# Kernel optimization log

Measured on AMD Instinct MI355X. Metric: run time of the kernel, lower is better.

## Reference

```python
import jax, jax.numpy as jnp
import numpy as np
import math

B, S, D, H, L, V, DFF = 16, 512, 1024, 16, 12, 32000, 4096
DK = D // H
MASK_ID = 1
LN_EPS = 1e-5


def _positional_encoding(seq_len, d):
    pos = np.arange(seq_len, dtype=np.float32)[:, None]
    div = np.exp(np.arange(0, d, 2, dtype=np.float32) * -(math.log(10000.0) / d))
    pe = np.zeros((seq_len, d), dtype=np.float32)
    pe[:, 0::2] = np.sin(pos * div)
    pe[:, 1::2] = np.cos(pos * div)
    return jnp.asarray(pe)


def _layernorm(x, scale, bias):
    mu = jnp.mean(x, axis=-1, keepdims=True)
    var = jnp.mean(jnp.square(x - mu), axis=-1, keepdims=True)
    return (x - mu) * jax.lax.rsqrt(var + LN_EPS) * scale + bias


def setup_inputs() -> dict:
    key = jax.random.key(0)
    ks = jax.random.split(key, 10)
    masked = jax.random.randint(ks[0], (B, S), 0, V, dtype=jnp.int32)
    tok_emb = jax.random.normal(ks[1], (V, D), dtype=jnp.float32) * 0.02
    tok_emb = tok_emb.at[0].set(0.0)  # padding_idx=0 row is zero
    seg_emb = jax.random.normal(ks[2], (3, D), dtype=jnp.float32) * 0.02
    return {
        "masked": masked,
        "tok_emb": tok_emb,
        "seg_emb": seg_emb,
        "ln1_scale": jnp.ones((L, D), jnp.float32),
        "ln1_bias": jnp.zeros((L, D), jnp.float32),
        "wq": jax.random.normal(ks[3], (L, D, D), dtype=jnp.float32) * 0.02,
        "bq": jnp.zeros((L, D), jnp.float32),
        "wo": jax.random.normal(ks[4], (L, D, D), dtype=jnp.float32) * 0.02,
        "bo": jnp.zeros((L, D), jnp.float32),
        "ln2_scale": jnp.ones((L, D), jnp.float32),
        "ln2_bias": jnp.zeros((L, D), jnp.float32),
        "w1": jax.random.normal(ks[5], (L, D, DFF), dtype=jnp.float32) * 0.02,
        "b1": jnp.zeros((L, DFF), jnp.float32),
        "w2": jax.random.normal(ks[6], (L, DFF, D), dtype=jnp.float32) * 0.02,
        "b2": jnp.zeros((L, D), jnp.float32),
    }


def reference(masked, tok_emb, seg_emb, ln1_scale, ln1_bias, wq, bq, wo, bo,
              ln2_scale, ln2_bias, w1, b1, w2, b2):
    pe = _positional_encoding(S, D)
    # segment_labels are forced to all-ones in the source forward
    x = tok_emb[masked] + pe[None, :, :] + seg_emb[1][None, None, :]  # [B,S,D]
    # pad mask built from (input != mask_id) as in source; broadcast over queries
    key_ok = (masked != MASK_ID)  # [B,S]
    attn_bias = jnp.where(key_ok[:, None, None, :], 0.0, -1e9)  # [B,1,1,S]
    scale = 1.0 / math.sqrt(DK)
    for l in range(L):
        xn = _layernorm(x, ln1_scale[l], ln1_bias[l])
        # NOTE: source uses q_linear for q, k and v -> single projection t
        t = (xn @ wq[l] + bq[l]).reshape(B, S, H, DK)
        scores = jnp.einsum("bqhd,bkhd->bhqk", t, t) * scale + attn_bias
        p = jax.nn.softmax(scores, axis=-1)
        o = jnp.einsum("bhqk,bkhd->bqhd", p, t).reshape(B, S, D)
        x = (o @ wo[l] + bo[l]) + x
        xn2 = _layernorm(x, ln2_scale[l], ln2_bias[l])
        h = jax.nn.gelu(xn2 @ w1[l] + b1[l], approximate=False)  # exact GELU (torch default)
        x = (h @ w2[l] + b2[l]) + x
    return x
```

## Files before the change

### kernel.cpp

```cpp
#include <hip/hip_runtime.h>


typedef unsigned short u16;
typedef unsigned int u32;
typedef short bf16x8 __attribute__((ext_vector_type(8)));
typedef float f32x4 __attribute__((ext_vector_type(4)));

__device__ __forceinline__ float bf2f(u16 u) {
    union { u32 i; float f; } v; v.i = ((u32)u) << 16; return v.f;
}
__device__ __forceinline__ u16 f2bf(float f) {
    union { float f; u32 i; } v; v.f = f;
    u32 r = v.i + 0x7fffu + ((v.i >> 16) & 1u);
    return (u16)(r >> 16);
}

__device__ __forceinline__ void gload16(const u16* g, u16* l) {
    __builtin_amdgcn_global_load_lds(
        (const __attribute__((address_space(1))) unsigned int*)g,
        (__attribute__((address_space(3))) unsigned int*)l, 16, 0, 0);
}

__global__ __launch_bounds__(256) void embed_kernel(
    const int* __restrict__ masked, const float* __restrict__ tok,
    const float* __restrict__ seg, float* __restrict__ x)
{
    int bs = blockIdx.x;
    int s  = bs & 511;
    int id = masked[bs];
    const float* te = tok + (size_t)id * 1024;
    float* xr = x + (size_t)bs * 1024;
    for (int d = threadIdx.x; d < 1024; d += 256) {
        int i2 = d & ~1;
        float ang = (float)s * expf((float)i2 * (-9.210340371976184f / 1024.0f));
        float pe  = (d & 1) ? cosf(ang) : sinf(ang);
        xr[d] = te[d] + pe + seg[1024 + d];
    }
}

__global__ __launch_bounds__(256) void ln_kernel(
    const float* __restrict__ x, const float* __restrict__ sc,
    const float* __restrict__ bi, u16* __restrict__ out)
{
    int row = blockIdx.x, tid = threadIdx.x;
    const float* xr = x + (size_t)row * 1024;
    float4 v = *(const float4*)&xr[tid * 4];
    float s = v.x + v.y + v.z + v.w;
    float q = v.x * v.x + v.y * v.y + v.z * v.z + v.w * v.w;
#pragma unroll
    for (int m = 1; m < 64; m <<= 1) { s += __shfl_xor(s, m); q += __shfl_xor(q, m); }
    __shared__ float rs[4], rq[4];
    int wave = tid >> 6, lane = tid & 63;
    if (lane == 0) { rs[wave] = s; rq[wave] = q; }
    __syncthreads();
    float ts = rs[0] + rs[1] + rs[2] + rs[3];
    float tq = rq[0] + rq[1] + rq[2] + rq[3];
    float mu = ts * (1.0f / 1024.0f);
    float var = tq * (1.0f / 1024.0f) - mu * mu;
    float rstd = rsqrtf(var + 1e-5f);
    u16* orow = out + (size_t)row * 1024;
    const float* vp = (const float*)&v;
#pragma unroll
    for (int j = 0; j < 4; ++j) {
        int c = tid * 4 + j;
        orow[c] = f2bf((vp[j] - mu) * rstd * sc[c] + bi[c]);
    }
}

__global__ __launch_bounds__(256) void transpose_f2b(
    const float* __restrict__ in, u16* __restrict__ out, int R, int C)
{
    __shared__ float tile[32][33];
    int bx = blockIdx.x * 32;
    int by = blockIdx.y * 32;
    int tx = threadIdx.x, ty = threadIdx.y;
#pragma unroll
    for (int i = 0; i < 4; ++i)
        tile[ty + i * 8][tx] = in[(size_t)(by + ty + i * 8) * C + bx + tx];
    __syncthreads();
#pragma unroll
    for (int i = 0; i < 4; ++i)
        out[(size_t)(bx + ty + i * 8) * R + by + tx] = f2bf(tile[tx][ty + i * 8]);
}

template <int MODE>
__global__ __launch_bounds__(256) void gemm_bt(
    const u16* __restrict__ A, const u16* __restrict__ BT,
    const float* __restrict__ bias, u16* __restrict__ Cb,
    float* __restrict__ Cf, int M, int N, int K)
{
    __shared__ u16 As[128 * 32];
    __shared__ u16 Bs[128 * 32];
    const int tid = threadIdx.x;
    const int wave = tid >> 6, lane = tid & 63;
    const int l16 = lane & 15, quad = lane >> 4;
    const int wm = (wave & 1) << 6, wn = (wave >> 1) << 6;
    const int tileM = blockIdx.x << 7, tileN = blockIdx.y << 7;
    const int r0 = tid >> 2, c0 = (tid & 3) << 3;

    const u16* Ag = A + (size_t)(tileM + r0) * K + c0;
    const u16* Bg = BT + (size_t)(tileN + r0) * K + c0;
    const size_t rowskip = (size_t)64 * K;
    u16* AsW  = As + wave * 512;
    u16* AsW2 = As + 2048 + wave * 512;
    u16* BsW  = Bs + wave * 512;
    u16* BsW2 = Bs + 2048 + wave * 512;

    f32x4 acc[4][4] = {};

    for (int k0 = 0; k0 < K; k0 += 32) {
        __syncthreads();
        gload16(Ag + k0,           AsW);
        gload16(Ag + k0 + rowskip, AsW2);
        gload16(Bg + k0,           BsW);
        gload16(Bg + k0 + rowskip, BsW2);
        __syncthreads();

        bf16x8 af[4], bfr[4];
#pragma unroll
        for (int i = 0; i < 4; ++i)
            af[i] = *(const bf16x8*)&As[(wm + i * 16 + l16) * 32 + quad * 8];
#pragma unroll
        for (int i = 0; i < 4; ++i)
            bfr[i] = *(const bf16x8*)&Bs[(wn + i * 16 + l16) * 32 + quad * 8];
#pragma unroll
        for (int mi = 0; mi < 4; ++mi)
#pragma unroll
            for (int ni = 0; ni < 4; ++ni)
                acc[mi][ni] = __builtin_amdgcn_mfma_f32_16x16x32_bf16(
                    af[mi], bfr[ni], acc[mi][ni], 0, 0, 0);
    }

    float bv[4];
#pragma unroll
    for (int ni = 0; ni < 4; ++ni) bv[ni] = bias[tileN + wn + ni * 16 + l16];
#pragma unroll
    for (int mi = 0; mi < 4; ++mi) {
        const int rbase = tileM + wm + mi * 16 + quad * 4;
#pragma unroll
        for (int ni = 0; ni < 4; ++ni) {
            const int col = tileN + wn + ni * 16 + l16;
#pragma unroll
            for (int r = 0; r < 4; ++r) {
                float v = acc[mi][ni][r] + bv[ni];
                size_t idx = (size_t)(rbase + r) * N + col;
                if (MODE == 0) {
                    Cb[idx] = f2bf(v);
                } else if (MODE == 1) {
                    float g = 0.5f * v * (1.0f + erff(v * 0.70710678118654752f));
                    Cb[idx] = f2bf(g);
                } else {
                    Cf[idx] += v;
                }
            }
        }
    }
}

__global__ __launch_bounds__(256) void attn_kernel(
    const u16* __restrict__ tt, const int* __restrict__ masked, u16* __restrict__ o)
{
    __shared__ float sbias[512];
    __shared__ u16 pT[4][512];
    const int bh = blockIdx.x;
    const int b = bh >> 4, h = bh & 15;
    const int qt = blockIdx.y;
    const int tid = threadIdx.x;
    const int wave = tid >> 6, lane = tid & 63;
    const int l16 = lane & 15, quad = lane >> 4;

    for (int i = tid; i < 512; i += 256)
        sbias[i] = (masked[b * 512 + i] == 1) ? -1e9f : 0.0f;
    __syncthreads();

    const size_t base = (size_t)b * 512 * 1024 + h * 64;
    const int q0 = qt * 64 + wave * 16;
    const u16* qrow = tt + base + (size_t)(q0 + l16) * 1024 + quad * 8;
    bf16x8 qf0 = *(const bf16x8*)qrow;
    bf16x8 qf1 = *(const bf16x8*)(qrow + 32);

    f32x4 oacc[4] = {};
    float lsum[4] = {0.f, 0.f, 0.f, 0.f};

    for (int kc = 0; kc < 16; ++kc) {
        const int k0 = kc * 32;
        f32x4 st[2];
#pragma unroll
        for (int nt = 0; nt < 2; ++nt) {
            const u16* krow = tt + base + (size_t)(k0 + nt * 16 + l16) * 1024 + quad * 8;
            bf16x8 kf0 = *(const bf16x8*)krow;
            bf16x8 kf1 = *(const bf16x8*)(krow + 32);
            f32x4 a = {};
            a = __builtin_amdgcn_mfma_f32_16x16x32_bf16(qf0, kf0, a, 0, 0, 0);
            a = __builtin_amdgcn_mfma_f32_16x16x32_bf16(qf1, kf1, a, 0, 0, 0);
            st[nt] = a;
        }
#pragma unroll
        for (int nt = 0; nt < 2; ++nt) {
            const float bvv = sbias[k0 + nt * 16 + l16];
#pragma unroll
            for (int r = 0; r < 4; ++r) {
                float p = expf(st[nt][r] * 0.125f + bvv);
                lsum[r] += p;
                pT[wave][(quad * 4 + r) * 32 + nt * 16 + l16] = f2bf(p);
            }
        }
        __syncthreads();
        bf16x8 pa = *(const bf16x8*)&pT[wave][l16 * 32 + quad * 8];
#pragma unroll
        for (int dt = 0; dt < 4; ++dt) {
            bf16x8 vf;
#pragma unroll
            for (int j = 0; j < 8; ++j)
                vf[j] = (short)tt[base + (size_t)(k0 + quad * 8 + j) * 1024 + dt * 16 + l16];
            oacc[dt] = __builtin_amdgcn_mfma_f32_16x16x32_bf16(pa, vf, oacc[dt], 0, 0, 0);
        }
        __syncthreads();
    }

#pragma unroll
    for (int r = 0; r < 4; ++r) {
        float s = lsum[r];
        s += __shfl_xor(s, 1);
        s += __shfl_xor(s, 2);
        s += __shfl_xor(s, 4);
        s += __shfl_xor(s, 8);
        lsum[r] = 1.0f / s;
    }
#pragma unroll
    for (int r = 0; r < 4; ++r) {
        const size_t orow = base + (size_t)(q0 + quad * 4 + r) * 1024;
#pragma unroll
        for (int dt = 0; dt < 4; ++dt)
            o[orow + dt * 16 + l16] = f2bf(oacc[dt][r] * lsum[r]);
    }
}

extern "C" void kernel_launch(void* const* d_in, const int* in_sizes, int n_in,
                              void* d_out, int out_size, void* d_ws, size_t ws_size,
                              hipStream_t stream)
{
    const int*   masked  = (const int*)d_in[0];
    const float* tok_emb = (const float*)d_in[1];
    const float* seg_emb = (const float*)d_in[2];
    const float* ln1_s   = (const float*)d_in[3];
    const float* ln1_b   = (const float*)d_in[4];
    const float* wq      = (const float*)d_in[5];
    const float* bq      = (const float*)d_in[6];
    const float* wo      = (const float*)d_in[7];
    const float* bo      = (const float*)d_in[8];
    const float* ln2_s   = (const float*)d_in[9];
    const float* ln2_b   = (const float*)d_in[10];
    const float* w1      = (const float*)d_in[11];
    const float* b1      = (const float*)d_in[12];
    const float* w2      = (const float*)d_in[13];
    const float* b2      = (const float*)d_in[14];
    float* out = (float*)d_out;

    char* p = (char*)d_ws;
    float* x  = (float*)p; p += (size_t)8192 * 1024 * 4;
    u16* xn   = (u16*)p;   p += (size_t)8192 * 1024 * 2;
    u16* tq   = (u16*)p;   p += (size_t)8192 * 1024 * 2;
    u16* ob   = (u16*)p;   p += (size_t)8192 * 1024 * 2;
    u16* hb   = (u16*)p;   p += (size_t)8192 * 4096 * 2;
    u16* wT   = (u16*)p;   p += (size_t)4096 * 1024 * 2;

    embed_kernel<<<8192, 256, 0, stream>>>(masked, tok_emb, seg_emb, x);

    for (int l = 0; l < 12; ++l) {
        const size_t oD  = (size_t)l * 1024;
        const size_t oF  = (size_t)l * 4096;
        const size_t oDD = (size_t)l * 1024 * 1024;
        const size_t oDF = (size_t)l * 1024 * 4096;

        ln_kernel<<<8192, 256, 0, stream>>>(x, ln1_s + oD, ln1_b + oD, xn);
        transpose_f2b<<<dim3(32, 32),  dim3(32, 8), 0, stream>>>(wq + oDD, wT, 1024, 1024);
        gemm_bt<0><<<dim3(64, 8), 256, 0, stream>>>(xn, wT, bq + oD, tq, nullptr, 8192, 1024, 1024);
        attn_kernel<<<dim3(256, 8), 256, 0, stream>>>(tq, masked, ob);
        transpose_f2b<<<dim3(32, 32),  dim3(32, 8), 0, stream>>>(wo + oDD, wT, 1024, 1024);
        gemm_bt<2><<<dim3(64, 8), 256, 0, stream>>>(ob, wT, bo + oD, nullptr, x, 8192, 1024, 1024);
        ln_kernel<<<8192, 256, 0, stream>>>(x, ln2_s + oD, ln2_b + oD, xn);
        transpose_f2b<<<dim3(128, 32), dim3(32, 8), 0, stream>>>(w1 + oDF, wT, 1024, 4096);
        gemm_bt<1><<<dim3(64, 32), 256, 0, stream>>>(xn, wT, b1 + oF, hb, nullptr, 8192, 4096, 1024);
        transpose_f2b<<<dim3(32, 128), dim3(32, 8), 0, stream>>>(w2 + oDF, wT, 4096, 1024);
        gemm_bt<2><<<dim3(64, 8), 256, 0, stream>>>(hb, wT, b2 + oD, nullptr, x, 8192, 1024, 4096);
    }

    hipMemcpyAsync(out, x, (size_t)8192 * 1024 * 4, hipMemcpyDeviceToDevice, stream);
}
```

Before: 5.597 ms.

## Double-buffer LDS tiles in bf16 GEMM to overlap loads with MFMA

Splits the shared-memory A and B tiles of the GEMM into two buffers. The loop is unrolled by two: the next k-slice is issued with async global-to-LDS loads while MFMAs run on the current buffer, and one barrier per slice replaces the two. This is meant to hide global load latency behind compute. It doubles LDS use per block, which can lower occupancy, and it assumes K is a multiple of 64.

```diff
diff --git a/kernel.cpp b/kernel.cpp
--- a/kernel.cpp
+++ b/kernel.cpp
@@ -89,8 +89,8 @@
     const float* __restrict__ bias, u16* __restrict__ Cb,
     float* __restrict__ Cf, int M, int N, int K)
 {
-    __shared__ u16 As[128 * 32];
-    __shared__ u16 Bs[128 * 32];
+    __shared__ u16 As[2][128 * 32];
+    __shared__ u16 Bs[2][128 * 32];
     const int tid = threadIdx.x;
     const int wave = tid >> 6, lane = tid & 63;
     const int l16 = lane & 15, quad = lane >> 4;
@@ -101,34 +101,41 @@
     const u16* Ag = A + (size_t)(tileM + r0) * K + c0;
     const u16* Bg = BT + (size_t)(tileN + r0) * K + c0;
     const size_t rowskip = (size_t)64 * K;
-    u16* AsW  = As + wave * 512;
-    u16* AsW2 = As + 2048 + wave * 512;
-    u16* BsW  = Bs + wave * 512;
-    u16* BsW2 = Bs + 2048 + wave * 512;
 
     f32x4 acc[4][4] = {};
 
-    for (int k0 = 0; k0 < K; k0 += 32) {
-        __syncthreads();
-        gload16(Ag + k0,           AsW);
-        gload16(Ag + k0 + rowskip, AsW2);
-        gload16(Bg + k0,           BsW);
-        gload16(Bg + k0 + rowskip, BsW2);
-        __syncthreads();
-
+    auto STAGE = [&](int buf, int kk) {
+        gload16(Ag + kk,           &As[buf][wave * 512]);
+        gload16(Ag + kk + rowskip, &As[buf][2048 + wave * 512]);
+        gload16(Bg + kk,           &Bs[buf][wave * 512]);
+        gload16(Bg + kk + rowskip, &Bs[buf][2048 + wave * 512]);
+    };
+    auto COMPUTE = [&](int buf) {
         bf16x8 af[4], bfr[4];
 #pragma unroll
         for (int i = 0; i < 4; ++i)
-            af[i] = *(const bf16x8*)&As[(wm + i * 16 + l16) * 32 + quad * 8];
+            af[i] = *(const bf16x8*)&As[buf][(wm + i * 16 + l16) * 32 + quad * 8];
 #pragma unroll
         for (int i = 0; i < 4; ++i)
-            bfr[i] = *(const bf16x8*)&Bs[(wn + i * 16 + l16) * 32 + quad * 8];
+            bfr[i] = *(const bf16x8*)&Bs[buf][(wn + i * 16 + l16) * 32 + quad * 8];
 #pragma unroll
         for (int mi = 0; mi < 4; ++mi)
 #pragma unroll
             for (int ni = 0; ni < 4; ++ni)
                 acc[mi][ni] = __builtin_amdgcn_mfma_f32_16x16x32_bf16(
                     af[mi], bfr[ni], acc[mi][ni], 0, 0, 0);
+    };
+
+    STAGE(0, 0);
+    __syncthreads();
+
+    for (int k0 = 0; k0 < K; k0 += 64) {
+        if (k0 + 32 < K) STAGE(1, k0 + 32);
+        COMPUTE(0);
+        __syncthreads();
+        if (k0 + 64 < K) STAGE(0, k0 + 64);
+        COMPUTE(1);
+        __syncthreads();
     }
 
     float bv[4];
```

Result: faster. 5.275 ms (-5.8%).
